# Kernel optimization log

Measured on AMD Instinct MI355X. Metric: run time of the kernel, lower is better.

The kernel has to match this reference:

```python
import jax, jax.numpy as jnp
import numpy as np

B, Q, K, D_IN, H, D_V = 4, 1024, 1024, 256, 64, 128
MASK_VAL = -1000000.0


def setup_inputs() -> dict:
    key = jax.random.key(0)
    k1, k2, k3, k4, k5, k6, k7 = jax.random.split(key, 7)
    queries = jax.random.normal(k1, (B, Q, D_IN), dtype=jnp.float32)
    keys = jax.random.normal(k2, (B, K, D_IN), dtype=jnp.float32)
    values = jax.random.normal(k3, (B, K, D_V), dtype=jnp.float32)
    valid_lens = jax.random.randint(k4, (B,), 1, K + 1)
    # Linear weights (no bias), stored as (in, out) for direct matmul
    W_q = jax.random.normal(k5, (D_IN, H), dtype=jnp.float32) / np.sqrt(D_IN)
    W_k = jax.random.normal(k6, (D_IN, H), dtype=jnp.float32) / np.sqrt(D_IN)
    w_v = jax.random.normal(k7, (H,), dtype=jnp.float32) / np.sqrt(H)
    return {"queries": queries, "keys": keys, "values": values,
            "valid_lens": valid_lens, "W_q": W_q, "W_k": W_k, "w_v": w_v}


def reference(queries, keys, values, valid_lens, W_q, W_k, w_v):
    # Project queries and keys to hidden dim H
    q = jnp.einsum("bqd,dh->bqh", queries, W_q)   # (B, Q, H)
    k = jnp.einsum("bkd,dh->bkh", keys, W_k)      # (B, K, H)
    # Additive (Bahdanau) scoring: broadcast-add + tanh + reduce over H
    feats = jnp.tanh(q[:, :, None, :] + k[:, None, :, :])   # (B, Q, K, H)
    scores = jnp.einsum("bqkh,h->bqk", feats, w_v)           # (B, Q, K)
    # Masked softmax over keys: positions >= valid_len get -1e6
    key_pos = jnp.arange(scores.shape[-1])                    # (K,)
    mask = key_pos[None, None, :] >= valid_lens[:, None, None]
    scores = jnp.where(mask, MASK_VAL, scores)
    attn = jax.nn.softmax(scores, axis=-1)                    # (B, Q, K)
    # Weighted sum of values (dropout is identity at rate 0.0 / eval)
    return jnp.einsum("bqk,bkv->bqv", attn, values)           # (B, Q, D_V)
```

## Files before the change

kernel.cpp:

```cpp
#include <hip/hip_runtime.h>
#include <hip/hip_fp16.h>
#include <math.h>

#define B_ 4
#define Q_ 1024
#define K_ 1024
#define DIN_ 256
#define H_ 64
#define DV_ 128
#define KT 64
#define MASKP -1000000.0f
#define C2LOG2E 2.8853900817779268f
#define LOG2E 1.4426950408889634f

__device__ __forceinline__ float fexp2(float x) {
#if __has_builtin(__builtin_amdgcn_exp2f)
  return __builtin_amdgcn_exp2f(x);
#else
  return exp2f(x);
#endif
}
__device__ __forceinline__ float frcp(float x) {
#if __has_builtin(__builtin_amdgcn_rcpf)
  return __builtin_amdgcn_rcpf(x);
#else
  return 1.0f / x;
#endif
}

__global__ __launch_bounds__(256, 4) void prep_kernel(
    const float* __restrict__ queries, const float* __restrict__ keys,
    const float* __restrict__ values,
    const float* __restrict__ Wq, const float* __restrict__ Wk,
    float* __restrict__ eq, float* __restrict__ ek,
    unsigned short* __restrict__ vh) {
  int bid = blockIdx.x;
  int t = threadIdx.x;
  if (bid >= 512) {
    int i = ((bid - 512) * 256 + t) * 4;
    float4 v = *(const float4*)&values[i];
    ushort4 o;
    o.x = __half_as_ushort(__float2half(v.x));
    o.y = __half_as_ushort(__float2half(v.y));
    o.z = __half_as_ushort(__float2half(v.z));
    o.w = __half_as_ushort(__float2half(v.w));
    *(ushort4*)&vh[i] = o;
    return;
  }
  int w = t >> 6, lane = t & 63;
  int r0 = __builtin_amdgcn_readfirstlane(bid * 16 + w * 4);
  const float* src;
  const float* W;
  float* dst;
  if (r0 < B_ * Q_) {
    src = queries + r0 * DIN_; W = Wq; dst = eq + r0 * H_;
  } else {
    int kr = r0 - B_ * Q_;
    src = keys + kr * DIN_; W = Wk; dst = ek + kr * H_;
  }
  float a00 = 0.f, a01 = 0.f, a10 = 0.f, a11 = 0.f;
  float a20 = 0.f, a21 = 0.f, a30 = 0.f, a31 = 0.f;
#pragma unroll 8
  for (int d = 0; d < DIN_; d += 2) {
    float w0 = W[d * H_ + lane];
    float w1 = W[(d + 1) * H_ + lane];
    a00 = fmaf(w0, src[d], a00);             a01 = fmaf(w1, src[d + 1], a01);
    a10 = fmaf(w0, src[DIN_ + d], a10);      a11 = fmaf(w1, src[DIN_ + d + 1], a11);
    a20 = fmaf(w0, src[2 * DIN_ + d], a20);  a21 = fmaf(w1, src[2 * DIN_ + d + 1], a21);
    a30 = fmaf(w0, src[3 * DIN_ + d], a30);  a31 = fmaf(w1, src[3 * DIN_ + d + 1], a31);
  }
  dst[lane]          = fexp2((a00 + a01) * C2LOG2E);
  dst[H_ + lane]     = fexp2((a10 + a11) * C2LOG2E);
  dst[2 * H_ + lane] = fexp2((a20 + a21) * C2LOG2E);
  dst[3 * H_ + lane] = fexp2((a30 + a31) * C2LOG2E);
}

__global__ __launch_bounds__(256, 4) void attn_kernel(
    const float* __restrict__ eq, const float* __restrict__ ek,
    const unsigned* __restrict__ vh32, const float* __restrict__ wv,
    const int* __restrict__ vlen,
    float* __restrict__ pl, float* __restrict__ po,
    int ns, int span) {
  __shared__ __align__(16) float ek_s[KT][H_ + 4];
  __shared__ __align__(16) unsigned v_s[KT][DV_ / 2];
  __shared__ __align__(16) float p_s[4][2][KT];
  __shared__ float4 eq4_s[8 * 16];
  __shared__ float4 wv4_s[16];
  int t = threadIdx.x;
  int lane = t & 63;
  int w = t >> 6;
  int b = blockIdx.x >> 7;
  int qt = blockIdx.x & 127;
  int s = blockIdx.y;
  int q0 = __builtin_amdgcn_readfirstlane(qt * 8 + w * 2);
  int kv = vlen[b];
  int g = b * Q_ + q0;
  int k_lo = s * span;

  if (k_lo >= kv) {
    if (lane == 0) {
      pl[(g + 0) * ns + s] = 0.f;
      pl[(g + 1) * ns + s] = 0.f;
    }
    return;
  }

  const float* ekb = ek + (size_t)b * K_ * H_;
  const unsigned* vgb = vh32 + (size_t)b * K_ * (DV_ / 2);

  if (t < 128)
    eq4_s[t] = ((const float4*)(eq + (size_t)(b * Q_ + qt * 8) * H_))[t];
  if (t < 16) wv4_s[t] = ((const float4*)wv)[t];

  float wsum = wv[lane];
#pragma unroll
  for (int sh = 32; sh >= 1; sh >>= 1) wsum += __shfl_xor(wsum, sh);
  float wl2 = wsum * LOG2E;
  const float nl2 = -2.0f * LOG2E;

  float l0 = 0.f, l1 = 0.f;
  float o0x = 0.f, o0y = 0.f, o1x = 0.f, o1y = 0.f;

  int tile0 = k_lo >> 6;
  int tileE = min((kv + KT - 1) >> 6, (k_lo + span) >> 6);
  const float4* e4a = &eq4_s[(w * 2 + 0) * 16];
  const float4* e4b = &eq4_s[(w * 2 + 1) * 16];

  for (int tile = tile0; tile < tileE; ++tile) {
    int k0 = tile * KT;
    __syncthreads();
    {
      const float4* gek = (const float4*)(ekb + (size_t)k0 * H_);
      const float4* gv = (const float4*)(vgb + (size_t)k0 * (DV_ / 2));
#pragma unroll
      for (int i = 0; i < 4; ++i) {
        int f4 = i * 256 + t;
        *(float4*)&ek_s[f4 >> 4][(f4 & 15) * 4] = gek[f4];
      }
#pragma unroll
      for (int i = 0; i < 4; ++i) {
        int f4 = i * 256 + t;
        *(float4*)&v_s[f4 >> 4][(f4 & 15) * 4] = gv[f4];
      }
    }
    __syncthreads();

    float acc0 = 0.f, acc1 = 0.f;
#pragma unroll
    for (int h4 = 0; h4 < 16; ++h4) {
      float4 ekv = *(const float4*)&ek_s[lane][h4 * 4];
      float4 wq = wv4_s[h4];
      float4 ea = e4a[h4];
      float4 eb = e4b[h4];
      {
        float d0 = fmaf(ea.x, ekv.x, 1.f), d1 = fmaf(ea.y, ekv.y, 1.f);
        acc0 = fmaf(fmaf(wq.y, d0, wq.x * d1), frcp(d0 * d1), acc0);
        float d2 = fmaf(ea.z, ekv.z, 1.f), d3 = fmaf(ea.w, ekv.w, 1.f);
        acc0 = fmaf(fmaf(wq.w, d2, wq.z * d3), frcp(d2 * d3), acc0);
      }
      {
        float d0 = fmaf(eb.x, ekv.x, 1.f), d1 = fmaf(eb.y, ekv.y, 1.f);
        acc1 = fmaf(fmaf(wq.y, d0, wq.x * d1), frcp(d0 * d1), acc1);
        float d2 = fmaf(eb.z, ekv.z, 1.f), d3 = fmaf(eb.w, ekv.w, 1.f);
        acc1 = fmaf(fmaf(wq.w, d2, wq.z * d3), frcp(d2 * d3), acc1);
      }
    }
    bool maskd = (k0 + lane) >= kv;
    float t0 = fmaf(nl2, acc0, wl2);
    float t1 = fmaf(nl2, acc1, wl2);
    if (maskd) { t0 = MASKP; t1 = MASKP; }
    float p0 = fexp2(t0), p1 = fexp2(t1);
    l0 += p0; l1 += p1;
    p_s[w][0][lane] = p0;
    p_s[w][1][lane] = p1;

#pragma unroll 8
    for (int k4 = 0; k4 < KT / 4; ++k4) {
      int kk = k4 * 4;
      float4 P0 = *(const float4*)&p_s[w][0][kk];
      float4 P1 = *(const float4*)&p_s[w][1][kk];
      unsigned u0 = v_s[kk][lane];
      unsigned u1 = v_s[kk + 1][lane];
      unsigned u2 = v_s[kk + 2][lane];
      unsigned u3 = v_s[kk + 3][lane];
      __half2 h0 = *(__half2*)&u0, h1 = *(__half2*)&u1;
      __half2 h2 = *(__half2*)&u2, h3 = *(__half2*)&u3;
      float v0x = __low2float(h0), v0y = __high2float(h0);
      float v1x = __low2float(h1), v1y = __high2float(h1);
      float v2x = __low2float(h2), v2y = __high2float(h2);
      float v3x = __low2float(h3), v3y = __high2float(h3);
      o0x = fmaf(P0.x, v0x, o0x); o0y = fmaf(P0.x, v0y, o0y);
      o1x = fmaf(P1.x, v0x, o1x); o1y = fmaf(P1.x, v0y, o1y);
      o0x = fmaf(P0.y, v1x, o0x); o0y = fmaf(P0.y, v1y, o0y);
      o1x = fmaf(P1.y, v1x, o1x); o1y = fmaf(P1.y, v1y, o1y);
      o0x = fmaf(P0.z, v2x, o0x); o0y = fmaf(P0.z, v2y, o0y);
      o1x = fmaf(P1.z, v2x, o1x); o1y = fmaf(P1.z, v2y, o1y);
      o0x = fmaf(P0.w, v3x, o0x); o0y = fmaf(P0.w, v3y, o0y);
      o1x = fmaf(P1.w, v3x, o1x); o1y = fmaf(P1.w, v3y, o1y);
    }
  }

#pragma unroll
  for (int sh = 32; sh >= 1; sh >>= 1) {
    l0 += __shfl_xor(l0, sh);
    l1 += __shfl_xor(l1, sh);
  }
  if (lane == 0) {
    pl[(g + 0) * ns + s] = l0;
    pl[(g + 1) * ns + s] = l1;
  }
  size_t pb = ((size_t)g * ns + s) * DV_ + lane * 2;
  *(float2*)&po[pb] = make_float2(o0x, o0y);
  *(float2*)&po[pb + (size_t)ns * DV_] = make_float2(o1x, o1y);
}

__global__ __launch_bounds__(256, 4) void combine_kernel(
    const float* __restrict__ pl, const float* __restrict__ po,
    float* __restrict__ out, int ns) {
  int t = threadIdx.x;
  int lane = t & 63;
  int w = t >> 6;
  int g = blockIdx.x * 4 + w;
  float L = 0.f, ax = 0.f, ay = 0.f;
  for (int s = 0; s < ns; ++s) {
    float ls = pl[g * ns + s];
    if (ls != 0.f) {
      L += ls;
      float2 o2 = *(const float2*)&po[((size_t)g * ns + s) * DV_ + lane * 2];
      ax += o2.x;
      ay += o2.y;
    }
  }
  float inv = frcp(L);
  *(float2*)&out[(size_t)g * DV_ + lane * 2] = make_float2(ax * inv, ay * inv);
}

extern "C" void kernel_launch(void* const* d_in, const int* in_sizes, int n_in,
                              void* d_out, int out_size, void* d_ws, size_t ws_size,
                              hipStream_t stream) {
  const float* queries = (const float*)d_in[0];
  const float* keys    = (const float*)d_in[1];
  const float* values  = (const float*)d_in[2];
  const int*   vl      = (const int*)d_in[3];
  const float* Wq      = (const float*)d_in[4];
  const float* Wk      = (const float*)d_in[5];
  const float* wv      = (const float*)d_in[6];
  float* out = (float*)d_out;

  float* eq = (float*)d_ws;
  float* ek = eq + (size_t)B_ * Q_ * H_;
  unsigned short* vh = (unsigned short*)(ek + (size_t)B_ * K_ * H_);
  char* dyn = (char*)(vh + (size_t)B_ * K_ * DV_);
  size_t fixed = (size_t)(dyn - (char*)d_ws);

  int ns = 2;
  for (int cand = 8; cand >= 2; cand >>= 1) {
    size_t need = fixed + (size_t)B_ * Q_ * cand * 4
                + (size_t)B_ * Q_ * cand * DV_ * 4;
    if (ws_size >= need) { ns = cand; break; }
  }
  int span = K_ / ns;
  float* pl = (float*)dyn;
  float* po = pl + (size_t)B_ * Q_ * ns;

  prep_kernel<<<dim3(1024), dim3(256), 0, stream>>>(
      queries, keys, values, Wq, Wk, eq, ek, vh);
  attn_kernel<<<dim3(B_ * (Q_ / 8), ns), dim3(256), 0, stream>>>(
      eq, ek, (const unsigned*)vh, wv, vl, pl, po, ns, span);
  combine_kernel<<<dim3(B_ * Q_ / 4), dim3(256), 0, stream>>>(pl, po, out, ns);
}
```

Baseline: 40.42 us.

## Merge tanh reciprocals into one per four and use packed FP32 FMAs

Pre-scales the exponentiated query features and the w_v weights by 2^-21 so each denominator term becomes eq*ek + 2^-21. This keeps products of four denominators in range, so a single reciprocal can serve four hidden elements instead of one per two. The denominator FMAs and the P·V accumulation are rewritten as two-wide float vector FMAs so the compiler can emit packed FP32 instructions on CDNA. The cost is a few extra multiplies per group and some risk of precision loss or overflow or underflow from the rescaling.

```diff
diff --git a/kernel.cpp b/kernel.cpp
--- a/kernel.cpp
+++ b/kernel.cpp
@@ -12,6 +12,9 @@
 #define MASKP -1000000.0f
 #define C2LOG2E 2.8853900817779268f
 #define LOG2E 1.4426950408889634f
+#define S21 4.76837158203125e-7f
+
+typedef float v2f __attribute__((ext_vector_type(2)));
 
 __device__ __forceinline__ float fexp2(float x) {
 #if __has_builtin(__builtin_amdgcn_exp2f)
@@ -52,11 +55,12 @@
   const float* src;
   const float* W;
   float* dst;
+  float escale;
   if (r0 < B_ * Q_) {
-    src = queries + r0 * DIN_; W = Wq; dst = eq + r0 * H_;
+    src = queries + r0 * DIN_; W = Wq; dst = eq + r0 * H_; escale = S21;
   } else {
     int kr = r0 - B_ * Q_;
-    src = keys + kr * DIN_; W = Wk; dst = ek + kr * H_;
+    src = keys + kr * DIN_; W = Wk; dst = ek + kr * H_; escale = 1.0f;
   }
   float a00 = 0.f, a01 = 0.f, a10 = 0.f, a11 = 0.f;
   float a20 = 0.f, a21 = 0.f, a30 = 0.f, a31 = 0.f;
@@ -69,10 +73,10 @@
     a20 = fmaf(w0, src[2 * DIN_ + d], a20);  a21 = fmaf(w1, src[2 * DIN_ + d + 1], a21);
     a30 = fmaf(w0, src[3 * DIN_ + d], a30);  a31 = fmaf(w1, src[3 * DIN_ + d + 1], a31);
   }
-  dst[lane]          = fexp2((a00 + a01) * C2LOG2E);
-  dst[H_ + lane]     = fexp2((a10 + a11) * C2LOG2E);
-  dst[2 * H_ + lane] = fexp2((a20 + a21) * C2LOG2E);
-  dst[3 * H_ + lane] = fexp2((a30 + a31) * C2LOG2E);
+  dst[lane]          = fexp2((a00 + a01) * C2LOG2E) * escale;
+  dst[H_ + lane]     = fexp2((a10 + a11) * C2LOG2E) * escale;
+  dst[2 * H_ + lane] = fexp2((a20 + a21) * C2LOG2E) * escale;
+  dst[3 * H_ + lane] = fexp2((a30 + a31) * C2LOG2E) * escale;
 }
 
 __global__ __launch_bounds__(256, 4) void attn_kernel(
@@ -110,7 +114,11 @@
 
   if (t < 128)
     eq4_s[t] = ((const float4*)(eq + (size_t)(b * Q_ + qt * 8) * H_))[t];
-  if (t < 16) wv4_s[t] = ((const float4*)wv)[t];
+  if (t < 16) {
+    float4 wq = ((const float4*)wv)[t];
+    wq.x *= S21; wq.y *= S21; wq.z *= S21; wq.w *= S21;
+    wv4_s[t] = wq;
+  }
 
   float wsum = wv[lane];
 #pragma unroll
@@ -119,12 +127,13 @@
   const float nl2 = -2.0f * LOG2E;
 
   float l0 = 0.f, l1 = 0.f;
-  float o0x = 0.f, o0y = 0.f, o1x = 0.f, o1y = 0.f;
+  v2f o0 = {0.f, 0.f}, o1 = {0.f, 0.f};
 
   int tile0 = k_lo >> 6;
   int tileE = min((kv + KT - 1) >> 6, (k_lo + span) >> 6);
   const float4* e4a = &eq4_s[(w * 2 + 0) * 16];
   const float4* e4b = &eq4_s[(w * 2 + 1) * 16];
+  const v2f c2 = {S21, S21};
 
   for (int tile = tile0; tile < tileE; ++tile) {
     int k0 = tile * KT;
@@ -148,21 +157,32 @@
     float acc0 = 0.f, acc1 = 0.f;
 #pragma unroll
     for (int h4 = 0; h4 < 16; ++h4) {
-      float4 ekv = *(const float4*)&ek_s[lane][h4 * 4];
+      float4 ekq = *(const float4*)&ek_s[lane][h4 * 4];
       float4 wq = wv4_s[h4];
       float4 ea = e4a[h4];
       float4 eb = e4b[h4];
+      v2f ek01 = {ekq.x, ekq.y}, ek23 = {ekq.z, ekq.w};
       {
-        float d0 = fmaf(ea.x, ekv.x, 1.f), d1 = fmaf(ea.y, ekv.y, 1.f);
-        acc0 = fmaf(fmaf(wq.y, d0, wq.x * d1), frcp(d0 * d1), acc0);
-        float d2 = fmaf(ea.z, ekv.z, 1.f), d3 = fmaf(ea.w, ekv.w, 1.f);
-        acc0 = fmaf(fmaf(wq.w, d2, wq.z * d3), frcp(d2 * d3), acc0);
+        v2f d01 = __builtin_elementwise_fma((v2f){ea.x, ea.y}, ek01, c2);
+        v2f d23 = __builtin_elementwise_fma((v2f){ea.z, ea.w}, ek23, c2);
+        float a01 = d01.x * d01.y;
+        float a23 = d23.x * d23.y;
+        float n01 = fmaf(wq.x, d01.y, wq.y * d01.x);
+        float n23 = fmaf(wq.z, d23.y, wq.w * d23.x);
+        float N = fmaf(n01, a23, n23 * a01);
+        float D = a01 * a23;
+        acc0 = fmaf(N, frcp(D), acc0);
       }
       {
-        float d0 = fmaf(eb.x, ekv.x, 1.f), d1 = fmaf(eb.y, ekv.y, 1.f);
-        acc1 = fmaf(fmaf(wq.y, d0, wq.x * d1), frcp(d0 * d1), acc1);
-        float d2 = fmaf(eb.z, ekv.z, 1.f), d3 = fmaf(eb.w, ekv.w, 1.f);
-        acc1 = fmaf(fmaf(wq.w, d2, wq.z * d3), frcp(d2 * d3), acc1);
+        v2f d01 = __builtin_elementwise_fma((v2f){eb.x, eb.y}, ek01, c2);
+        v2f d23 = __builtin_elementwise_fma((v2f){eb.z, eb.w}, ek23, c2);
+        float a01 = d01.x * d01.y;
+        float a23 = d23.x * d23.y;
+        float n01 = fmaf(wq.x, d01.y, wq.y * d01.x);
+        float n23 = fmaf(wq.z, d23.y, wq.w * d23.x);
+        float N = fmaf(n01, a23, n23 * a01);
+        float D = a01 * a23;
+        acc1 = fmaf(N, frcp(D), acc1);
       }
     }
     bool maskd = (k0 + lane) >= kv;
@@ -185,18 +205,18 @@
       unsigned u3 = v_s[kk + 3][lane];
       __half2 h0 = *(__half2*)&u0, h1 = *(__half2*)&u1;
       __half2 h2 = *(__half2*)&u2, h3 = *(__half2*)&u3;
-      float v0x = __low2float(h0), v0y = __high2float(h0);
-      float v1x = __low2float(h1), v1y = __high2float(h1);
-      float v2x = __low2float(h2), v2y = __high2float(h2);
-      float v3x = __low2float(h3), v3y = __high2float(h3);
-      o0x = fmaf(P0.x, v0x, o0x); o0y = fmaf(P0.x, v0y, o0y);
-      o1x = fmaf(P1.x, v0x, o1x); o1y = fmaf(P1.x, v0y, o1y);
-      o0x = fmaf(P0.y, v1x, o0x); o0y = fmaf(P0.y, v1y, o0y);
-      o1x = fmaf(P1.y, v1x, o1x); o1y = fmaf(P1.y, v1y, o1y);
-      o0x = fmaf(P0.z, v2x, o0x); o0y = fmaf(P0.z, v2y, o0y);
-      o1x = fmaf(P1.z, v2x, o1x); o1y = fmaf(P1.z, v2y, o1y);
-      o0x = fmaf(P0.w, v3x, o0x); o0y = fmaf(P0.w, v3y, o0y);
-      o1x = fmaf(P1.w, v3x, o1x); o1y = fmaf(P1.w, v3y, o1y);
+      v2f v0 = {__low2float(h0), __high2float(h0)};
+      v2f v1 = {__low2float(h1), __high2float(h1)};
+      v2f v2 = {__low2float(h2), __high2float(h2)};
+      v2f v3 = {__low2float(h3), __high2float(h3)};
+      o0 = __builtin_elementwise_fma((v2f){P0.x, P0.x}, v0, o0);
+      o1 = __builtin_elementwise_fma((v2f){P1.x, P1.x}, v0, o1);
+      o0 = __builtin_elementwise_fma((v2f){P0.y, P0.y}, v1, o0);
+      o1 = __builtin_elementwise_fma((v2f){P1.y, P1.y}, v1, o1);
+      o0 = __builtin_elementwise_fma((v2f){P0.z, P0.z}, v2, o0);
+      o1 = __builtin_elementwise_fma((v2f){P1.z, P1.z}, v2, o1);
+      o0 = __builtin_elementwise_fma((v2f){P0.w, P0.w}, v3, o0);
+      o1 = __builtin_elementwise_fma((v2f){P1.w, P1.w}, v3, o1);
     }
   }
 
@@ -210,8 +230,8 @@
     pl[(g + 1) * ns + s] = l1;
   }
   size_t pb = ((size_t)g * ns + s) * DV_ + lane * 2;
-  *(float2*)&po[pb] = make_float2(o0x, o0y);
-  *(float2*)&po[pb + (size_t)ns * DV_] = make_float2(o1x, o1y);
+  *(float2*)&po[pb] = make_float2(o0.x, o0.y);
+  *(float2*)&po[pb + (size_t)ns * DV_] = make_float2(o1.x, o1.y);
 }
 
 __global__ __launch_bounds__(256, 4) void combine_kernel(
```

New measurement: 41.01 us. No clear change (+1.4%).

## Store exponentiated key projections as fp16 to halve LDS and global traffic

Applied to the files above, without the earlier changes.

The prep kernel now writes exp(2k) for the keys as clamped fp16 instead of fp32. The attention kernel stages these as packed half2 words in a smaller shared tile and converts them to float inside the score loop. Launch bounds rise to 5 blocks per CU to exploit the lower LDS footprint. This cuts global and LDS bandwidth and raises occupancy, at the cost of fp16 rounding and clamping at 60000 on the key factor, plus extra conversion instructions in the hot loop.

```diff
diff --git a/kernel.cpp b/kernel.cpp
--- a/kernel.cpp
+++ b/kernel.cpp
@@ -12,6 +12,7 @@
 #define MASKP -1000000.0f
 #define C2LOG2E 2.8853900817779268f
 #define LOG2E 1.4426950408889634f
+#define EKMAX 60000.0f
 
 __device__ __forceinline__ float fexp2(float x) {
 #if __has_builtin(__builtin_amdgcn_exp2f)
@@ -32,7 +33,7 @@
     const float* __restrict__ queries, const float* __restrict__ keys,
     const float* __restrict__ values,
     const float* __restrict__ Wq, const float* __restrict__ Wk,
-    float* __restrict__ eq, float* __restrict__ ek,
+    float* __restrict__ eq, unsigned short* __restrict__ ekh,
     unsigned short* __restrict__ vh) {
   int bid = blockIdx.x;
   int t = threadIdx.x;
@@ -49,15 +50,11 @@
   }
   int w = t >> 6, lane = t & 63;
   int r0 = __builtin_amdgcn_readfirstlane(bid * 16 + w * 4);
+  bool isq = (r0 < B_ * Q_);
   const float* src;
   const float* W;
-  float* dst;
-  if (r0 < B_ * Q_) {
-    src = queries + r0 * DIN_; W = Wq; dst = eq + r0 * H_;
-  } else {
-    int kr = r0 - B_ * Q_;
-    src = keys + kr * DIN_; W = Wk; dst = ek + kr * H_;
-  }
+  if (isq) { src = queries + r0 * DIN_; W = Wq; }
+  else     { src = keys + (r0 - B_ * Q_) * DIN_; W = Wk; }
   float a00 = 0.f, a01 = 0.f, a10 = 0.f, a11 = 0.f;
   float a20 = 0.f, a21 = 0.f, a30 = 0.f, a31 = 0.f;
 #pragma unroll 8
@@ -69,19 +66,30 @@
     a20 = fmaf(w0, src[2 * DIN_ + d], a20);  a21 = fmaf(w1, src[2 * DIN_ + d + 1], a21);
     a30 = fmaf(w0, src[3 * DIN_ + d], a30);  a31 = fmaf(w1, src[3 * DIN_ + d + 1], a31);
   }
-  dst[lane]          = fexp2((a00 + a01) * C2LOG2E);
-  dst[H_ + lane]     = fexp2((a10 + a11) * C2LOG2E);
-  dst[2 * H_ + lane] = fexp2((a20 + a21) * C2LOG2E);
-  dst[3 * H_ + lane] = fexp2((a30 + a31) * C2LOG2E);
-}
-
-__global__ __launch_bounds__(256, 4) void attn_kernel(
-    const float* __restrict__ eq, const float* __restrict__ ek,
+  float e0 = fexp2((a00 + a01) * C2LOG2E);
+  float e1 = fexp2((a10 + a11) * C2LOG2E);
+  float e2 = fexp2((a20 + a21) * C2LOG2E);
+  float e3 = fexp2((a30 + a31) * C2LOG2E);
+  if (isq) {
+    float* dst = eq + r0 * H_;
+    dst[lane] = e0; dst[H_ + lane] = e1;
+    dst[2 * H_ + lane] = e2; dst[3 * H_ + lane] = e3;
+  } else {
+    unsigned short* dst = ekh + (r0 - B_ * Q_) * H_;
+    dst[lane]          = __half_as_ushort(__float2half(fminf(e0, EKMAX)));
+    dst[H_ + lane]     = __half_as_ushort(__float2half(fminf(e1, EKMAX)));
+    dst[2 * H_ + lane] = __half_as_ushort(__float2half(fminf(e2, EKMAX)));
+    dst[3 * H_ + lane] = __half_as_ushort(__float2half(fminf(e3, EKMAX)));
+  }
+}
+
+__global__ __launch_bounds__(256, 5) void attn_kernel(
+    const float* __restrict__ eq, const unsigned short* __restrict__ ekh,
     const unsigned* __restrict__ vh32, const float* __restrict__ wv,
     const int* __restrict__ vlen,
     float* __restrict__ pl, float* __restrict__ po,
     int ns, int span) {
-  __shared__ __align__(16) float ek_s[KT][H_ + 4];
+  __shared__ __align__(16) unsigned ek_s[KT][H_ / 2 + 2];
   __shared__ __align__(16) unsigned v_s[KT][DV_ / 2];
   __shared__ __align__(16) float p_s[4][2][KT];
   __shared__ float4 eq4_s[8 * 16];
@@ -105,7 +113,7 @@
     return;
   }
 
-  const float* ekb = ek + (size_t)b * K_ * H_;
+  const unsigned short* ekb = ekh + (size_t)b * K_ * H_;
   const unsigned* vgb = vh32 + (size_t)b * K_ * (DV_ / 2);
 
   if (t < 128)
@@ -131,12 +139,15 @@
     __syncthreads();
     {
       const float4* gek = (const float4*)(ekb + (size_t)k0 * H_);
+#pragma unroll
+      for (int i = 0; i < 2; ++i) {
+        int f4 = i * 256 + t;
+        float4 v = gek[f4];
+        int r = f4 >> 3, c = (f4 & 7) * 4;
+        *(float2*)&ek_s[r][c] = make_float2(v.x, v.y);
+        *(float2*)&ek_s[r][c + 2] = make_float2(v.z, v.w);
+      }
       const float4* gv = (const float4*)(vgb + (size_t)k0 * (DV_ / 2));
-#pragma unroll
-      for (int i = 0; i < 4; ++i) {
-        int f4 = i * 256 + t;
-        *(float4*)&ek_s[f4 >> 4][(f4 & 15) * 4] = gek[f4];
-      }
 #pragma unroll
       for (int i = 0; i < 4; ++i) {
         int f4 = i * 256 + t;
@@ -145,24 +156,40 @@
     }
     __syncthreads();
 
+    const unsigned* ekrow = ek_s[lane];
     float acc0 = 0.f, acc1 = 0.f;
 #pragma unroll
-    for (int h4 = 0; h4 < 16; ++h4) {
-      float4 ekv = *(const float4*)&ek_s[lane][h4 * 4];
-      float4 wq = wv4_s[h4];
-      float4 ea = e4a[h4];
-      float4 eb = e4b[h4];
+    for (int h8 = 0; h8 < 8; ++h8) {
+      uint2 eu0 = *(const uint2*)&ekrow[h8 * 4];
+      uint2 eu1 = *(const uint2*)&ekrow[h8 * 4 + 2];
+      __half2 eh0 = *(__half2*)&eu0.x, eh1 = *(__half2*)&eu0.y;
+      __half2 eh2 = *(__half2*)&eu1.x, eh3 = *(__half2*)&eu1.y;
+      float k0f = __low2float(eh0), k1f = __high2float(eh0);
+      float k2f = __low2float(eh1), k3f = __high2float(eh1);
+      float k4f = __low2float(eh2), k5f = __high2float(eh2);
+      float k6f = __low2float(eh3), k7f = __high2float(eh3);
+      float4 wqA = wv4_s[h8 * 2], wqB = wv4_s[h8 * 2 + 1];
+      float4 eaA = e4a[h8 * 2], eaB = e4a[h8 * 2 + 1];
+      float4 ebA = e4b[h8 * 2], ebB = e4b[h8 * 2 + 1];
       {
-        float d0 = fmaf(ea.x, ekv.x, 1.f), d1 = fmaf(ea.y, ekv.y, 1.f);
-        acc0 = fmaf(fmaf(wq.y, d0, wq.x * d1), frcp(d0 * d1), acc0);
-        float d2 = fmaf(ea.z, ekv.z, 1.f), d3 = fmaf(ea.w, ekv.w, 1.f);
-        acc0 = fmaf(fmaf(wq.w, d2, wq.z * d3), frcp(d2 * d3), acc0);
+        float d0 = fmaf(eaA.x, k0f, 1.f), d1 = fmaf(eaA.y, k1f, 1.f);
+        acc0 = fmaf(fmaf(wqA.y, d0, wqA.x * d1), frcp(d0 * d1), acc0);
+        float d2 = fmaf(eaA.z, k2f, 1.f), d3 = fmaf(eaA.w, k3f, 1.f);
+        acc0 = fmaf(fmaf(wqA.w, d2, wqA.z * d3), frcp(d2 * d3), acc0);
+        float d4 = fmaf(eaB.x, k4f, 1.f), d5 = fmaf(eaB.y, k5f, 1.f);
+        acc0 = fmaf(fmaf(wqB.y, d4, wqB.x * d5), frcp(d4 * d5), acc0);
+        float d6 = fmaf(eaB.z, k6f, 1.f), d7 = fmaf(eaB.w, k7f, 1.f);
+        acc0 = fmaf(fmaf(wqB.w, d6, wqB.z * d7), frcp(d6 * d7), acc0);
       }
       {
-        float d0 = fmaf(eb.x, ekv.x, 1.f), d1 = fmaf(eb.y, ekv.y, 1.f);
-        acc1 = fmaf(fmaf(wq.y, d0, wq.x * d1), frcp(d0 * d1), acc1);
-        float d2 = fmaf(eb.z, ekv.z, 1.f), d3 = fmaf(eb.w, ekv.w, 1.f);
-        acc1 = fmaf(fmaf(wq.w, d2, wq.z * d3), frcp(d2 * d3), acc1);
+        float d0 = fmaf(ebA.x, k0f, 1.f), d1 = fmaf(ebA.y, k1f, 1.f);
+        acc1 = fmaf(fmaf(wqA.y, d0, wqA.x * d1), frcp(d0 * d1), acc1);
+        float d2 = fmaf(ebA.z, k2f, 1.f), d3 = fmaf(ebA.w, k3f, 1.f);
+        acc1 = fmaf(fmaf(wqA.w, d2, wqA.z * d3), frcp(d2 * d3), acc1);
+        float d4 = fmaf(ebB.x, k4f, 1.f), d5 = fmaf(ebB.y, k5f, 1.f);
+        acc1 = fmaf(fmaf(wqB.y, d4, wqB.x * d5), frcp(d4 * d5), acc1);
+        float d6 = fmaf(ebB.z, k6f, 1.f), d7 = fmaf(ebB.w, k7f, 1.f);
+        acc1 = fmaf(fmaf(wqB.w, d6, wqB.z * d7), frcp(d6 * d7), acc1);
       }
     }
     bool maskd = (k0 + lane) >= kv;
@@ -248,8 +275,8 @@
   float* out = (float*)d_out;
 
   float* eq = (float*)d_ws;
-  float* ek = eq + (size_t)B_ * Q_ * H_;
-  unsigned short* vh = (unsigned short*)(ek + (size_t)B_ * K_ * H_);
+  unsigned short* ekh = (unsigned short*)(eq + (size_t)B_ * Q_ * H_);
+  unsigned short* vh = ekh + (size_t)B_ * K_ * H_;
   char* dyn = (char*)(vh + (size_t)B_ * K_ * DV_);
   size_t fixed = (size_t)(dyn - (char*)d_ws);
 
@@ -264,8 +291,8 @@
   float* po = pl + (size_t)B_ * Q_ * ns;
 
   prep_kernel<<<dim3(1024), dim3(256), 0, stream>>>(
-      queries, keys, values, Wq, Wk, eq, ek, vh);
+      queries, keys, values, Wq, Wk, eq, ekh, vh);
   attn_kernel<<<dim3(B_ * (Q_ / 8), ns), dim3(256), 0, stream>>>(
-      eq, ek, (const unsigned*)vh, wv, vl, pl, po, ns, span);
+      eq, ekh, (const unsigned*)vh, wv, vl, pl, po, ns, span);
   combine_kernel<<<dim3(B_ * Q_ / 4), dim3(256), 0, stream>>>(pl, po, out, ns);
 }
```

New measurement: 38.71 us. 4.2% less time.
